# Kernel tuning notes

Hardware: AMD Instinct MI355X
Metric: run time of the kernel (lower is better)

The kernel has to match this reference:

```python
import jax, jax.numpy as jnp
import numpy as np

M, N, K = 35637, 15872, 20
FEAT = 128
EPS = 1e-5
W0 = 1.0  # Sine frequency


def setup_inputs() -> dict:
    key = jax.random.key(0)
    ks = jax.random.split(key, 8)
    x_feat = jax.random.normal(ks[0], (1, N, FEAT), dtype=jnp.float32)
    w_up_inputs = jax.random.uniform(ks[1], (1, 7, M, K), dtype=jnp.float32)
    idx = jax.random.randint(ks[2], (1, M, K), 0, N - 1)
    conv0_w = jax.random.normal(ks[3], (128, 7), dtype=jnp.float32) * (1.0 / np.sqrt(7))
    convs_w = jax.random.normal(ks[4], (7, 128, 128), dtype=jnp.float32) * (1.0 / np.sqrt(128))
    gammas = jnp.ones((8, 128), dtype=jnp.float32)
    betas = jnp.zeros((8, 128), dtype=jnp.float32)
    final_w = jax.random.normal(ks[5], (1, 128), dtype=jnp.float32) * (1.0 / np.sqrt(128))
    final_b = jnp.zeros((1,), dtype=jnp.float32)
    return {"x_feat": x_feat, "w_up_inputs": w_up_inputs, "idx": idx,
            "conv0_w": conv0_w, "convs_w": convs_w, "gammas": gammas,
            "betas": betas, "final_w": final_w, "final_b": final_b}


def _conv_bn_sine(h, W, g, b):
    # 1x1 conv == per-point matmul over channel dim; h: (B, M, K, Cin)
    h = jnp.einsum('bmkc,oc->bmko', h, W)
    # BatchNorm2d in training mode: batch stats over (B, M, K) per channel
    mu = jnp.mean(h, axis=(0, 1, 2))
    var = jnp.var(h, axis=(0, 1, 2))
    h = (h - mu) * jax.lax.rsqrt(var + EPS) * g + b
    return jnp.sin(W0 * h)


def reference(x_feat, w_up_inputs, idx, conv0_w, convs_w, gammas, betas, final_w, final_b):
    # w_up_inputs: (B, 7, M, K) -> channels-last (B, M, K, 7)
    h = jnp.transpose(w_up_inputs, (0, 2, 3, 1))
    h = _conv_bn_sine(h, conv0_w, gammas[0], betas[0])
    for i in range(7):
        h = _conv_bn_sine(h, convs_w[i], gammas[i + 1], betas[i + 1])
    # final 1x1 conv with bias -> logits (B, M, K, 1)
    logits = jnp.einsum('bmkc,oc->bmko', h, final_w) + final_b
    w = jax.nn.softmax(logits, axis=2)  # softmax over K neighbors
    # index_points: gather x_feat[b, idx[b, m, k], :] -> (B, M, K, FEAT)
    gathered = jax.vmap(lambda pts, ix: pts[ix])(x_feat, idx)
    feat_H = jnp.sum(w * gathered, axis=2)  # (B, M, FEAT)
    return feat_H
```

## Files before the change

kernel.cpp:

```cpp
#include <hip/hip_runtime.h>

#define PP 712740
#define MM 35637
#define KK 20
#define NF 15872
#define NTILES 44547
#define NSUPER 11137
#define ZROWS (NSUPER * 64)

typedef _Float16 h16;
typedef __attribute__((ext_vector_type(8))) _Float16 f16x8;
typedef __attribute__((ext_vector_type(4))) float f32x4;

__global__ __launch_bounds__(256) void k_zero(double* __restrict__ gs) {
  const int t = threadIdx.x;
#pragma unroll
  for (int i = 0; i < 8; ++i) gs[i * 256 + t] = 0.0;
}

__global__ __launch_bounds__(256) void k_stats0(
    const float* __restrict__ up,
    const float* __restrict__ w0,
    double* __restrict__ gs)
{
  __shared__ float w0s[128 * 7];
  __shared__ double red[4][256];
  const int t = threadIdx.x;
  for (int i = t; i < 128 * 7; i += 256) w0s[i] = (float)(h16)w0[i];
  __syncthreads();

  const int w = t >> 6;
  const int lane = t & 63;
  const int ln = lane & 15;
  const int q = lane >> 4;

  float sp[32], qp[32];
#pragma unroll
  for (int i = 0; i < 32; ++i) { sp[i] = 0.f; qp[i] = 0.f; }

  const int gw = blockIdx.x * 4 + w;
  for (int tile = gw; tile < NTILES; tile += gridDim.x * 4) {
    const int p = tile * 16 + ln;
    const bool act = p < PP;
    float u[7];
#pragma unroll
    for (int c7 = 0; c7 < 7; ++c7) u[c7] = act ? up[(size_t)c7 * PP + p] : 0.f;

#pragma unroll
    for (int ks = 0; ks < 4; ++ks)
#pragma unroll
      for (int j = 0; j < 8; ++j) {
        const int c = ks * 32 + q * 8 + j;
        float acc = 0.f;
#pragma unroll
        for (int c7 = 0; c7 < 7; ++c7) acc = fmaf(w0s[c * 7 + c7], u[c7], acc);
        const int si = ks * 8 + j;
        sp[si] += acc;
        qp[si] = fmaf(acc, acc, qp[si]);
      }
  }

#pragma unroll
  for (int i = 0; i < 32; ++i) {
#pragma unroll
    for (int d = 1; d < 16; d <<= 1) {
      sp[i] += __shfl_xor(sp[i], d, 64);
      qp[i] += __shfl_xor(qp[i], d, 64);
    }
  }
  if (ln == 0) {
#pragma unroll
    for (int ks = 0; ks < 4; ++ks)
#pragma unroll
      for (int j = 0; j < 8; ++j) {
        const int c = ks * 32 + q * 8 + j;
        red[w][c] = (double)sp[ks * 8 + j];
        red[w][128 + c] = (double)qp[ks * 8 + j];
      }
  }
  __syncthreads();
  double v = red[0][t] + red[1][t] + red[2][t] + red[3][t];
  atomicAdd(&gs[t], v);
}

__global__ __launch_bounds__(256, 3) void k_layer1(
    const float* __restrict__ up,
    const float* __restrict__ w0,
    h16* __restrict__ zout,
    const double* __restrict__ gsp,
    double* __restrict__ gso,
    const float* __restrict__ W,
    const float* __restrict__ gamma,
    const float* __restrict__ beta)
{
  __shared__ h16 actA[8192];
  __shared__ h16 actB[8192];
  __shared__ double red[256];

  const int t = threadIdx.x;
  const int w = t >> 6;
  const int lane = t & 63;
  const int ln = lane & 15;
  const int q = lane >> 4;
  const int G = (int)gridDim.x;

  float sc[8], sh[8];
  {
    const double n = (double)PP;
    const int cb = (t & 15) * 8;
#pragma unroll
    for (int j = 0; j < 8; ++j) {
      const int c = cb + j;
      const double mu = gsp[c] / n;
      const double var = gsp[128 + c] / n - mu * mu;
      const float rstd = (float)(1.0 / sqrt(var + 1e-5));
      sc[j] = rstd * gamma[c];
      sh[j] = beta[c] - (float)mu * sc[j];
    }
  }

  h16 w0h[7][8];
  {
    const int cb = (t & 15) * 8;
#pragma unroll
    for (int c7 = 0; c7 < 7; ++c7)
#pragma unroll
      for (int j = 0; j < 8; ++j)
        w0h[c7][j] = (h16)w0[(cb + j) * 7 + c7];
  }

  const int ob = w * 32;
  f16x8 wfr[2][4];
#pragma unroll
  for (int nt = 0; nt < 2; ++nt) {
    const int row_g = ob + (ln >> 2) * 8 + nt * 4 + (ln & 3);
    const float* wrow = W + (size_t)row_g * 128;
#pragma unroll
    for (int ks = 0; ks < 4; ++ks) {
      const float* src = wrow + ks * 32 + q * 8;
      const float4 aa = *(const float4*)src;
      const float4 bb = *(const float4*)(src + 4);
      f16x8 b;
      b[0] = (h16)aa.x; b[1] = (h16)aa.y; b[2] = (h16)aa.z; b[3] = (h16)aa.w;
      b[4] = (h16)bb.x; b[5] = (h16)bb.y; b[6] = (h16)bb.z; b[7] = (h16)bb.w;
      wfr[nt][ks] = b;
    }
  }

  float sp[8], qp[8];
#pragma unroll
  for (int i = 0; i < 8; ++i) { sp[i] = 0.f; qp[i] = 0.f; }

  const int wbase = (t >> 4) * 256 + (((t & 15) ^ ((t >> 4) & 7)) << 4);
  int raddr[4];
#pragma unroll
  for (int ks = 0; ks < 4; ++ks)
    raddr[ks] = ln * 256 + (((ks * 4 + q) ^ (ln & 7)) << 4);
  const int obase = ln * 256 + (((w * 4 + q) ^ (ln & 7)) << 4);
  const int rbase = (t >> 4) * 256 + (((t & 15) ^ ((t >> 4) & 7)) << 4);

  char* A = (char*)actA;
  char* B = (char*)actB;

  for (int stile = blockIdx.x; stile < NSUPER; stile += G) {
    float u[4][7];
#pragma unroll
    for (int s = 0; s < 4; ++s) {
      const int p = stile * 64 + (t >> 4) + 16 * s;
      const bool act = p < PP;
#pragma unroll
      for (int c7 = 0; c7 < 7; ++c7)
        u[s][c7] = act ? up[(size_t)c7 * PP + p] : 0.f;
    }

#pragma unroll
    for (int s = 0; s < 4; ++s) {
      f16x8 av;
#pragma unroll
      for (int j = 0; j < 8; ++j) {
        float acc = 0.f;
#pragma unroll
        for (int c7 = 0; c7 < 7; ++c7)
          acc = fmaf((float)w0h[c7][j], u[s][c7], acc);
        av[j] = (h16)__sinf(fmaf(acc, sc[j], sh[j]));
      }
      *(f16x8*)(A + (wbase + s * 4096)) = av;
    }

    asm volatile("s_waitcnt lgkmcnt(0)\n\ts_barrier" ::: "memory");

#pragma unroll
    for (int ot = 0; ot < 4; ++ot) {
      f16x8 afr[4];
#pragma unroll
      for (int ks = 0; ks < 4; ++ks)
        afr[ks] = *(const f16x8*)(A + (ot * 4096 + raddr[ks]));

      f32x4 acc0 = (f32x4){0.f, 0.f, 0.f, 0.f};
      f32x4 acc1 = (f32x4){0.f, 0.f, 0.f, 0.f};
#pragma unroll
      for (int ks = 0; ks < 4; ++ks) {
        acc0 = __builtin_amdgcn_mfma_f32_16x16x32_f16(wfr[0][ks], afr[ks], acc0, 0, 0, 0);
        acc1 = __builtin_amdgcn_mfma_f32_16x16x32_f16(wfr[1][ks], afr[ks], acc1, 0, 0, 0);
      }

      const int p = stile * 64 + ot * 16 + ln;
      if (p < PP) {
#pragma unroll
        for (int r = 0; r < 4; ++r) {
          sp[r]     += acc0[r];
          qp[r]      = fmaf(acc0[r], acc0[r], qp[r]);
          sp[4 + r] += acc1[r];
          qp[4 + r]  = fmaf(acc1[r], acc1[r], qp[4 + r]);
        }
      }
      f16x8 o;
      o[0] = (h16)acc0[0]; o[1] = (h16)acc0[1]; o[2] = (h16)acc0[2]; o[3] = (h16)acc0[3];
      o[4] = (h16)acc1[0]; o[5] = (h16)acc1[1]; o[6] = (h16)acc1[2]; o[7] = (h16)acc1[3];
      *(f16x8*)(B + (ot * 4096 + obase)) = o;
    }

    asm volatile("s_waitcnt lgkmcnt(0)\n\ts_barrier" ::: "memory");

    {
      const size_t zo = (size_t)stile * 8192;
#pragma unroll
      for (int pass = 0; pass < 4; ++pass) {
        const f16x8 v = *(const f16x8*)(B + (pass * 4096 + rbase));
        *(f16x8*)(zout + zo + (size_t)pass * 2048 + (size_t)t * 8) = v;
      }
    }
  }

#pragma unroll
  for (int i = 0; i < 8; ++i) {
#pragma unroll
    for (int d = 1; d < 16; d <<= 1) {
      sp[i] += __shfl_xor(sp[i], d, 64);
      qp[i] += __shfl_xor(qp[i], d, 64);
    }
  }
  if (ln == 0) {
#pragma unroll
    for (int r = 0; r < 4; ++r) {
      const int c = ob + q * 8 + r;
      red[c]           = (double)sp[r];
      red[c + 4]       = (double)sp[4 + r];
      red[128 + c]     = (double)qp[r];
      red[128 + c + 4] = (double)qp[4 + r];
    }
  }
  __syncthreads();
  atomicAdd(&gso[t], red[t]);
}

__global__ __launch_bounds__(256, 4) void k_layer(
    const h16* zin,
    h16* zout,
    const double* __restrict__ gsp,
    double* __restrict__ gso,
    const float* __restrict__ W,
    const float* __restrict__ gamma,
    const float* __restrict__ beta)
{
  __shared__ h16 actA[8192];
  __shared__ h16 actB[8192];
  __shared__ double red[256];

  const int t = threadIdx.x;
  const int w = t >> 6;
  const int lane = t & 63;
  const int ln = lane & 15;
  const int q = lane >> 4;
  const int G = (int)gridDim.x;

  float sc[8], sh[8];
  {
    const double n = (double)PP;
    const int cb = (t & 15) * 8;
#pragma unroll
    for (int j = 0; j < 8; ++j) {
      const int c = cb + j;
      const double mu = gsp[c] / n;
      const double var = gsp[128 + c] / n - mu * mu;
      const float rstd = (float)(1.0 / sqrt(var + 1e-5));
      sc[j] = rstd * gamma[c];
      sh[j] = beta[c] - (float)mu * sc[j];
    }
  }

  const int ob = w * 32;
  f16x8 wfr[2][4];
#pragma unroll
  for (int nt = 0; nt < 2; ++nt) {
    const int row_g = ob + (ln >> 2) * 8 + nt * 4 + (ln & 3);
    const float* wrow = W + (size_t)row_g * 128;
#pragma unroll
    for (int ks = 0; ks < 4; ++ks) {
      const float* src = wrow + ks * 32 + q * 8;
      const float4 aa = *(const float4*)src;
      const float4 bb = *(const float4*)(src + 4);
      f16x8 b;
      b[0] = (h16)aa.x; b[1] = (h16)aa.y; b[2] = (h16)aa.z; b[3] = (h16)aa.w;
      b[4] = (h16)bb.x; b[5] = (h16)bb.y; b[6] = (h16)bb.z; b[7] = (h16)bb.w;
      wfr[nt][ks] = b;
    }
  }

  float sp[8], qp[8];
#pragma unroll
  for (int i = 0; i < 8; ++i) { sp[i] = 0.f; qp[i] = 0.f; }

  const size_t roff = (size_t)(t >> 4) * 128 + (size_t)(t & 15) * 8;
  const int wbase = (t >> 4) * 256 + (((t & 15) ^ ((t >> 4) & 7)) << 4);
  int raddr[4];
#pragma unroll
  for (int ks = 0; ks < 4; ++ks)
    raddr[ks] = ln * 256 + (((ks * 4 + q) ^ (ln & 7)) << 4);
  const int obase = ln * 256 + (((w * 4 + q) ^ (ln & 7)) << 4);
  const int rbase = (t >> 4) * 256 + (((t & 15) ^ ((t >> 4) & 7)) << 4);

  int stile = blockIdx.x;
  f16x8 raw[4];
  {
    const h16* src = zin + (size_t)stile * 8192 + roff;
#pragma unroll
    for (int s = 0; s < 4; ++s) raw[s] = *(const f16x8*)(src + s * 2048);
  }

  char* A = (char*)actA;
  char* B = (char*)actB;

  for (; stile < NSUPER; stile += G) {
#pragma unroll
    for (int s = 0; s < 4; ++s) {
      f16x8 av;
#pragma unroll
      for (int j = 0; j < 8; ++j)
        av[j] = (h16)__sinf(fmaf((float)raw[s][j], sc[j], sh[j]));
      *(f16x8*)(A + (wbase + s * 4096)) = av;
    }

    {
      const int nxt = (stile + G < NSUPER) ? stile + G : NSUPER - 1;
      const h16* src = zin + (size_t)nxt * 8192 + roff;
#pragma unroll
      for (int s = 0; s < 4; ++s) raw[s] = *(const f16x8*)(src + s * 2048);
    }

    asm volatile("s_waitcnt lgkmcnt(0)\n\ts_barrier" ::: "memory");

#pragma unroll
    for (int ot = 0; ot < 4; ++ot) {
      f16x8 afr[4];
#pragma unroll
      for (int ks = 0; ks < 4; ++ks)
        afr[ks] = *(const f16x8*)(A + (ot * 4096 + raddr[ks]));

      f32x4 acc0 = (f32x4){0.f, 0.f, 0.f, 0.f};
      f32x4 acc1 = (f32x4){0.f, 0.f, 0.f, 0.f};
#pragma unroll
      for (int ks = 0; ks < 4; ++ks) {
        acc0 = __builtin_amdgcn_mfma_f32_16x16x32_f16(wfr[0][ks], afr[ks], acc0, 0, 0, 0);
        acc1 = __builtin_amdgcn_mfma_f32_16x16x32_f16(wfr[1][ks], afr[ks], acc1, 0, 0, 0);
      }

      const int p = stile * 64 + ot * 16 + ln;
      if (p < PP) {
#pragma unroll
        for (int r = 0; r < 4; ++r) {
          sp[r]     += acc0[r];
          qp[r]      = fmaf(acc0[r], acc0[r], qp[r]);
          sp[4 + r] += acc1[r];
          qp[4 + r]  = fmaf(acc1[r], acc1[r], qp[4 + r]);
        }
      }
      f16x8 o;
      o[0] = (h16)acc0[0]; o[1] = (h16)acc0[1]; o[2] = (h16)acc0[2]; o[3] = (h16)acc0[3];
      o[4] = (h16)acc1[0]; o[5] = (h16)acc1[1]; o[6] = (h16)acc1[2]; o[7] = (h16)acc1[3];
      *(f16x8*)(B + (ot * 4096 + obase)) = o;
    }

    asm volatile("s_waitcnt lgkmcnt(0)\n\ts_barrier" ::: "memory");

    {
      const size_t zo = (size_t)stile * 8192;
#pragma unroll
      for (int pass = 0; pass < 4; ++pass) {
        const f16x8 v = *(const f16x8*)(B + (pass * 4096 + rbase));
        *(f16x8*)(zout + zo + (size_t)pass * 2048 + (size_t)t * 8) = v;
      }
    }
  }

#pragma unroll
  for (int i = 0; i < 8; ++i) {
#pragma unroll
    for (int d = 1; d < 16; d <<= 1) {
      sp[i] += __shfl_xor(sp[i], d, 64);
      qp[i] += __shfl_xor(qp[i], d, 64);
    }
  }
  if (ln == 0) {
#pragma unroll
    for (int r = 0; r < 4; ++r) {
      const int c = ob + q * 8 + r;
      red[c]           = (double)sp[r];
      red[c + 4]       = (double)sp[4 + r];
      red[128 + c]     = (double)qp[r];
      red[128 + c + 4] = (double)qp[4 + r];
    }
  }
  __syncthreads();
  atomicAdd(&gso[t], red[t]);
}

__global__ __launch_bounds__(256) void k_outf(
    const h16* __restrict__ z,
    const double* __restrict__ gsp,
    const float* __restrict__ gamma,
    const float* __restrict__ beta,
    const float* __restrict__ fw,
    const float* __restrict__ fb,
    const int* __restrict__ idx,
    const float* __restrict__ xf,
    float* __restrict__ out)
{
  const int gw = (int)((blockIdx.x * 256 + threadIdx.x) >> 6);
  const int lane = (int)(threadIdx.x & 63);
  if (gw >= MM) return;
  const int m = gw;
  const int ln = lane & 15;
  const int q = lane >> 4;
  const int c0 = ln * 8;

  float scv[8], shv[8], fv[8];
#pragma unroll
  for (int j = 0; j < 8; ++j) {
    const int c = c0 + j;
    const double n = (double)PP;
    const double mu = gsp[c] / n;
    const double var = gsp[128 + c] / n - mu * mu;
    const float rstd = (float)(1.0 / sqrt(var + 1e-5));
    scv[j] = rstd * gamma[c];
    shv[j] = beta[c] - (float)mu * scv[j];
    fv[j] = fw[c];
  }
  const float fbv = fb[0];

  float lg[5];
#pragma unroll
  for (int g = 0; g < 5; ++g) {
    const h16* zp = z + (size_t)(m * KK + g * 4 + q) * 128 + c0;
    const f16x8 raw = *(const f16x8*)zp;
    float part = 0.f;
#pragma unroll
    for (int j = 0; j < 8; ++j)
      part = fmaf(fv[j], __sinf(fmaf((float)raw[j], scv[j], shv[j])), part);
    part += __shfl_xor(part, 1, 64);
    part += __shfl_xor(part, 2, 64);
    part += __shfl_xor(part, 4, 64);
    part += __shfl_xor(part, 8, 64);
    lg[g] = part + fbv;
  }

  float l1[5], l2[5], l3[5];
#pragma unroll
  for (int g = 0; g < 5; ++g) {
    l1[g] = __shfl_xor(lg[g], 16, 64);
    l2[g] = __shfl_xor(lg[g], 32, 64);
    l3[g] = __shfl_xor(l1[g], 32, 64);
  }

  float mx = lg[0];
#pragma unroll
  for (int g = 0; g < 5; ++g) {
    mx = fmaxf(mx, lg[g]); mx = fmaxf(mx, l1[g]);
    mx = fmaxf(mx, l2[g]); mx = fmaxf(mx, l3[g]);
  }
  float w0e[5], w1e[5], w2e[5], w3e[5];
  float ssum = 0.f;
#pragma unroll
  for (int g = 0; g < 5; ++g) {
    w0e[g] = __expf(lg[g] - mx); ssum += w0e[g];
    w1e[g] = __expf(l1[g] - mx); ssum += w1e[g];
    w2e[g] = __expf(l2[g] - mx); ssum += w2e[g];
    w3e[g] = __expf(l3[g] - mx); ssum += w3e[g];
  }
  const float inv = 1.f / ssum;

  float a0 = 0.f, a1 = 0.f;
#pragma unroll
  for (int g = 0; g < 5; ++g) {
#pragma unroll
    for (int e = 0; e < 4; ++e) {
      const int k = 4 * g + (q ^ e);
      const float we = (e == 0 ? w0e[g] : e == 1 ? w1e[g] : e == 2 ? w2e[g] : w3e[g]);
      const int r = idx[m * KK + k];
      const float wk = we * inv;
      a0 = fmaf(wk, xf[r * 128 + lane], a0);
      a1 = fmaf(wk, xf[r * 128 + 64 + lane], a1);
    }
  }
  out[m * 128 + lane] = a0;
  out[m * 128 + 64 + lane] = a1;
}

__global__ __launch_bounds__(256) void k_out(
    const float* __restrict__ logits,
    const int* __restrict__ idx,
    const float* __restrict__ xf,
    float* __restrict__ out)
{
  const int gw = (int)((blockIdx.x * 256 + threadIdx.x) >> 6);
  const int lane = threadIdx.x & 63;
  if (gw >= MM) return;
  const int m = gw;

  float l[KK];
#pragma unroll
  for (int k = 0; k < KK; ++k) l[k] = logits[m * KK + k];
  float mx = l[0];
#pragma unroll
  for (int k = 1; k < KK; ++k) mx = fmaxf(mx, l[k]);
  float ssum = 0.f;
#pragma unroll
  for (int k = 0; k < KK; ++k) { l[k] = __expf(l[k] - mx); ssum += l[k]; }
  const float inv = 1.f / ssum;

  float a0 = 0.f, a1 = 0.f;
#pragma unroll
  for (int k = 0; k < KK; ++k) {
    const int r = idx[m * KK + k];
    const float wk = l[k] * inv;
    a0 = fmaf(wk, xf[r * 128 + lane], a0);
    a1 = fmaf(wk, xf[r * 128 + 64 + lane], a1);
  }
  out[m * 128 + lane] = a0;
  out[m * 128 + 64 + lane] = a1;
}

__global__ __launch_bounds__(256) void k_chain(
    const float* __restrict__ up,
    const float* __restrict__ w0,
    const float* __restrict__ wc,
    const float* __restrict__ gam,
    const float* __restrict__ bet,
    const double* __restrict__ gs,
    double* __restrict__ gso,
    int jl, int mode,
    const float* __restrict__ fw,
    const float* __restrict__ fb,
    float* __restrict__ logits)
{
  __shared__ float sc_s[8][128], sh_s[8][128];
  __shared__ double bred[4][256];
  const int t = threadIdx.x;
  const int lane = t & 63;

  const int nbn = (mode == 0) ? jl : 8;
  for (int i = t; i < nbn * 128; i += 256) {
    const int L = i >> 7, c = i & 127;
    const double n = (double)PP;
    const double mu = gs[L * 256 + c] / n;
    const double var = gs[L * 256 + 128 + c] / n - mu * mu;
    const float rstd = (float)(1.0 / sqrt(var + 1e-5));
    const float sc = rstd * gam[L * 128 + c];
    sc_s[L][c] = sc;
    sh_s[L][c] = bet[L * 128 + c] - (float)mu * sc;
  }
  __syncthreads();

  double lS0 = 0, lS1 = 0, lQ0 = 0, lQ1 = 0;

  for (int p0 = blockIdx.x * 256; p0 < PP; p0 += gridDim.x * 256) {
    const int p = p0 + t;
    const bool act = p < PP;

    float a[128];
    {
      float u[7];
#pragma unroll
      for (int c = 0; c < 7; ++c) u[c] = act ? up[c * PP + p] : 0.f;
#pragma unroll 1
      for (int och = 0; och < 16; ++och) {
#pragma unroll
        for (int j = 0; j < 8; ++j) {
          float acc = 0.f;
#pragma unroll
          for (int c = 0; c < 7; ++c)
            acc = fmaf(w0[(och * 8 + j) * 7 + c], u[c], acc);
          a[och * 8 + j] = acc;
        }
      }
    }

#pragma unroll 1
    for (int L = 0; L < jl; ++L) {
#pragma unroll
      for (int c = 0; c < 128; ++c)
        a[c] = act ? __sinf(fmaf(a[c], sc_s[L][c], sh_s[L][c])) : 0.f;
      float b[128];
      const float* W = wc + (size_t)L * 128 * 128;
#pragma unroll 1
      for (int och = 0; och < 16; ++och) {
#pragma unroll
        for (int j = 0; j < 8; ++j) {
          float acc = 0.f;
#pragma unroll
          for (int c = 0; c < 128; ++c)
            acc = fmaf(W[(och * 8 + j) * 128 + c], a[c], acc);
          b[och * 8 + j] = acc;
        }
      }
#pragma unroll
      for (int c = 0; c < 128; ++c) a[c] = b[c];
    }

    if (mode == 0) {
#pragma unroll
      for (int o = 0; o < 128; ++o) {
        float s = a[o];
        float qv = a[o] * a[o];
#pragma unroll
        for (int d = 32; d > 0; d >>= 1) {
          s += __shfl_xor(s, d, 64);
          qv += __shfl_xor(qv, d, 64);
        }
        if ((o & 63) == lane) {
          if (o < 64) { lS0 += (double)s; lQ0 += (double)qv; }
          else        { lS1 += (double)s; lQ1 += (double)qv; }
        }
      }
    } else if (act) {
      float acc = fb[0];
#pragma unroll
      for (int c = 0; c < 128; ++c) {
        const float h = fmaf(a[c], sc_s[7][c], sh_s[7][c]);
        acc = fmaf(fw[c], __sinf(h), acc);
      }
      logits[p] = acc;
    }
  }

  if (mode == 0) {
    const int w = t >> 6;
    bred[w][lane]       = lS0;
    bred[w][64 + lane]  = lS1;
    bred[w][128 + lane] = lQ0;
    bred[w][192 + lane] = lQ1;
    __syncthreads();
    double v = bred[0][t] + bred[1][t] + bred[2][t] + bred[3][t];
    atomicAdd(&gso[t], v);
  }
}

extern "C" void kernel_launch(void* const* d_in, const int* in_sizes, int n_in,
                              void* d_out, int out_size, void* d_ws, size_t ws_size,
                              hipStream_t stream) {
  const float* xf  = (const float*)d_in[0];
  const float* up  = (const float*)d_in[1];
  const int*   idx = (const int*)d_in[2];
  const float* w0  = (const float*)d_in[3];
  const float* wc  = (const float*)d_in[4];
  const float* gam = (const float*)d_in[5];
  const float* bet = (const float*)d_in[6];
  const float* fw  = (const float*)d_in[7];
  const float* fb  = (const float*)d_in[8];
  float* out = (float*)d_out;

  char* ws = (char*)d_ws;
  const size_t zb     = (size_t)ZROWS * 128 * sizeof(h16);
  const size_t statsb = 8 * 256 * sizeof(double);
  const int NB = 1024;
  const int nbo = (MM + 3) / 4;

  if (ws_size >= zb + statsb) {
    h16* z = (h16*)ws;
    double* gs = (double*)(ws + zb);

    k_zero<<<1, 256, 0, stream>>>(gs);
    k_stats0<<<NB, 256, 0, stream>>>(up, w0, gs);
    k_layer1<<<NB, 256, 0, stream>>>(up, w0, z, gs, gs + 256,
                                     wc, gam, bet);
    for (int i = 2; i <= 7; ++i) {
      k_layer<<<NB, 256, 0, stream>>>(z, z,
                                      gs + (size_t)(i - 1) * 256,
                                      gs + (size_t)i * 256,
                                      wc + (size_t)(i - 1) * 128 * 128,
                                      gam + (size_t)(i - 1) * 128,
                                      bet + (size_t)(i - 1) * 128);
    }
    k_outf<<<nbo, 256, 0, stream>>>(z, gs + 7 * 256, gam + 7 * 128,
                                    bet + 7 * 128, fw, fb, idx, xf, out);
  } else {
    double* gs = (double*)ws;
    float* logits = (float*)(ws + statsb);

    k_zero<<<1, 256, 0, stream>>>(gs);
    for (int j = 0; j <= 7; ++j) {
      k_chain<<<NB, 256, 0, stream>>>(up, w0, wc, gam, bet, gs,
                                      gs + (size_t)j * 256, j, 0,
                                      fw, fb, logits);
    }
    k_chain<<<NB, 256, 0, stream>>>(up, w0, wc, gam, bet, gs,
                                    nullptr, 7, 1, fw, fb, logits);
    k_out<<<nbo, 256, 0, stream>>>(logits, idx, xf, out);
  }
}
```

Before: 708.6 us.

## Replace last layer write-back with stats-only pass plus recompute-to-logits pass

The final conv layer no longer writes its fp16 activations back to the workspace. One kernel computes the layer-7 matmul only to gather batch-norm statistics. A second kernel recomputes the same matmul, applies BN, sine and the final projection in registers, and writes only per-point logits. The existing k_out kernel then does the softmax and gather. This removes a full 712k×128 fp16 write and its later reread, at the cost of running the last matmul twice and launching one extra kernel.

```diff
diff --git a/kernel.cpp b/kernel.cpp
--- a/kernel.cpp
+++ b/kernel.cpp
@@ -415,95 +415,292 @@
   atomicAdd(&gso[t], red[t]);
 }
 
-__global__ __launch_bounds__(256) void k_outf(
-    const h16* __restrict__ z,
+__global__ __launch_bounds__(256, 4) void k_stats7(
+    const h16* __restrict__ zin,
     const double* __restrict__ gsp,
+    double* __restrict__ gso,
+    const float* __restrict__ W,
     const float* __restrict__ gamma,
-    const float* __restrict__ beta,
+    const float* __restrict__ beta)
+{
+  __shared__ h16 actA[8192];
+  __shared__ double red[256];
+
+  const int t = threadIdx.x;
+  const int w = t >> 6;
+  const int lane = t & 63;
+  const int ln = lane & 15;
+  const int q = lane >> 4;
+  const int G = (int)gridDim.x;
+
+  float sc[8], sh[8];
+  {
+    const double n = (double)PP;
+    const int cb = (t & 15) * 8;
+#pragma unroll
+    for (int j = 0; j < 8; ++j) {
+      const int c = cb + j;
+      const double mu = gsp[c] / n;
+      const double var = gsp[128 + c] / n - mu * mu;
+      const float rstd = (float)(1.0 / sqrt(var + 1e-5));
+      sc[j] = rstd * gamma[c];
+      sh[j] = beta[c] - (float)mu * sc[j];
+    }
+  }
+
+  const int ob = w * 32;
+  f16x8 wfr[2][4];
+#pragma unroll
+  for (int nt = 0; nt < 2; ++nt) {
+    const int row_g = ob + (ln >> 2) * 8 + nt * 4 + (ln & 3);
+    const float* wrow = W + (size_t)row_g * 128;
+#pragma unroll
+    for (int ks = 0; ks < 4; ++ks) {
+      const float* src = wrow + ks * 32 + q * 8;
+      const float4 aa = *(const float4*)src;
+      const float4 bb = *(const float4*)(src + 4);
+      f16x8 b;
+      b[0] = (h16)aa.x; b[1] = (h16)aa.y; b[2] = (h16)aa.z; b[3] = (h16)aa.w;
+      b[4] = (h16)bb.x; b[5] = (h16)bb.y; b[6] = (h16)bb.z; b[7] = (h16)bb.w;
+      wfr[nt][ks] = b;
+    }
+  }
+
+  float sp[8], qp[8];
+#pragma unroll
+  for (int i = 0; i < 8; ++i) { sp[i] = 0.f; qp[i] = 0.f; }
+
+  const size_t roff = (size_t)(t >> 4) * 128 + (size_t)(t & 15) * 8;
+  const int wbase = (t >> 4) * 256 + (((t & 15) ^ ((t >> 4) & 7)) << 4);
+  int raddr[4];
+#pragma unroll
+  for (int ks = 0; ks < 4; ++ks)
+    raddr[ks] = ln * 256 + (((ks * 4 + q) ^ (ln & 7)) << 4);
+
+  int stile = blockIdx.x;
+  f16x8 raw[4];
+  {
+    const h16* src = zin + (size_t)stile * 8192 + roff;
+#pragma unroll
+    for (int s = 0; s < 4; ++s) raw[s] = *(const f16x8*)(src + s * 2048);
+  }
+
+  char* A = (char*)actA;
+
+  for (; stile < NSUPER; stile += G) {
+#pragma unroll
+    for (int s = 0; s < 4; ++s) {
+      f16x8 av;
+#pragma unroll
+      for (int j = 0; j < 8; ++j)
+        av[j] = (h16)__sinf(fmaf((float)raw[s][j], sc[j], sh[j]));
+      *(f16x8*)(A + (wbase + s * 4096)) = av;
+    }
+
+    {
+      const int nxt = (stile + G < NSUPER) ? stile + G : NSUPER - 1;
+      const h16* src = zin + (size_t)nxt * 8192 + roff;
+#pragma unroll
+      for (int s = 0; s < 4; ++s) raw[s] = *(const f16x8*)(src + s * 2048);
+    }
+
+    asm volatile("s_waitcnt lgkmcnt(0)\n\ts_barrier" ::: "memory");
+
+#pragma unroll
+    for (int ot = 0; ot < 4; ++ot) {
+      f16x8 afr[4];
+#pragma unroll
+      for (int ks = 0; ks < 4; ++ks)
+        afr[ks] = *(const f16x8*)(A + (ot * 4096 + raddr[ks]));
+
+      f32x4 acc0 = (f32x4){0.f, 0.f, 0.f, 0.f};
+      f32x4 acc1 = (f32x4){0.f, 0.f, 0.f, 0.f};
+#pragma unroll
+      for (int ks = 0; ks < 4; ++ks) {
+        acc0 = __builtin_amdgcn_mfma_f32_16x16x32_f16(wfr[0][ks], afr[ks], acc0, 0, 0, 0);
+        acc1 = __builtin_amdgcn_mfma_f32_16x16x32_f16(wfr[1][ks], afr[ks], acc1, 0, 0, 0);
+      }
+
+      const int p = stile * 64 + ot * 16 + ln;
+      if (p < PP) {
+#pragma unroll
+        for (int r = 0; r < 4; ++r) {
+          sp[r]     += acc0[r];
+          qp[r]      = fmaf(acc0[r], acc0[r], qp[r]);
+          sp[4 + r] += acc1[r];
+          qp[4 + r]  = fmaf(acc1[r], acc1[r], qp[4 + r]);
+        }
+      }
+    }
+
+    asm volatile("s_waitcnt lgkmcnt(0)\n\ts_barrier" ::: "memory");
+  }
+
+#pragma unroll
+  for (int i = 0; i < 8; ++i) {
+#pragma unroll
+    for (int d = 1; d < 16; d <<= 1) {
+      sp[i] += __shfl_xor(sp[i], d, 64);
+      qp[i] += __shfl_xor(qp[i], d, 64);
+    }
+  }
+  if (ln == 0) {
+#pragma unroll
+    for (int r = 0; r < 4; ++r) {
+      const int c = ob + q * 8 + r;
+      red[c]           = (double)sp[r];
+      red[c + 4]       = (double)sp[4 + r];
+      red[128 + c]     = (double)qp[r];
+      red[128 + c + 4] = (double)qp[4 + r];
+    }
+  }
+  __syncthreads();
+  atomicAdd(&gso[t], red[t]);
+}
+
+__global__ __launch_bounds__(256, 3) void k_logits7(
+    const h16* __restrict__ zin,
+    const double* __restrict__ gspA,
+    const float* __restrict__ gamA,
+    const float* __restrict__ betA,
+    const float* __restrict__ W,
+    const double* __restrict__ gspO,
+    const float* __restrict__ gamO,
+    const float* __restrict__ betO,
     const float* __restrict__ fw,
     const float* __restrict__ fb,
-    const int* __restrict__ idx,
-    const float* __restrict__ xf,
-    float* __restrict__ out)
+    float* __restrict__ logits)
 {
-  const int gw = (int)((blockIdx.x * 256 + threadIdx.x) >> 6);
-  const int lane = (int)(threadIdx.x & 63);
-  if (gw >= MM) return;
-  const int m = gw;
+  __shared__ h16 actA[8192];
+  __shared__ float lf[4][64];
+
+  const int t = threadIdx.x;
+  const int w = t >> 6;
+  const int lane = t & 63;
   const int ln = lane & 15;
   const int q = lane >> 4;
-  const int c0 = ln * 8;
-
-  float scv[8], shv[8], fv[8];
-#pragma unroll
-  for (int j = 0; j < 8; ++j) {
-    const int c = c0 + j;
+  const int G = (int)gridDim.x;
+
+  float sc[8], sh[8];
+  {
     const double n = (double)PP;
-    const double mu = gsp[c] / n;
-    const double var = gsp[128 + c] / n - mu * mu;
-    const float rstd = (float)(1.0 / sqrt(var + 1e-5));
-    scv[j] = rstd * gamma[c];
-    shv[j] = beta[c] - (float)mu * scv[j];
-    fv[j] = fw[c];
+    const int cb = (t & 15) * 8;
+#pragma unroll
+    for (int j = 0; j < 8; ++j) {
+      const int c = cb + j;
+      const double mu = gspA[c] / n;
+      const double var = gspA[128 + c] / n - mu * mu;
+      const float rstd = (float)(1.0 / sqrt(var + 1e-5));
+      sc[j] = rstd * gamA[c];
+      sh[j] = betA[c] - (float)mu * sc[j];
+    }
+  }
+
+  const int ob = w * 32;
+  float scO[8], shO[8], fwO[8];
+  {
+    const double n = (double)PP;
+    const int cb = ob + q * 8;
+#pragma unroll
+    for (int j = 0; j < 8; ++j) {
+      const int c = cb + j;
+      const double mu = gspO[c] / n;
+      const double var = gspO[128 + c] / n - mu * mu;
+      const float rstd = (float)(1.0 / sqrt(var + 1e-5));
+      scO[j] = rstd * gamO[c];
+      shO[j] = betO[c] - (float)mu * scO[j];
+      fwO[j] = fw[c];
+    }
   }
   const float fbv = fb[0];
 
-  float lg[5];
-#pragma unroll
-  for (int g = 0; g < 5; ++g) {
-    const h16* zp = z + (size_t)(m * KK + g * 4 + q) * 128 + c0;
-    const f16x8 raw = *(const f16x8*)zp;
-    float part = 0.f;
-#pragma unroll
-    for (int j = 0; j < 8; ++j)
-      part = fmaf(fv[j], __sinf(fmaf((float)raw[j], scv[j], shv[j])), part);
-    part += __shfl_xor(part, 1, 64);
-    part += __shfl_xor(part, 2, 64);
-    part += __shfl_xor(part, 4, 64);
-    part += __shfl_xor(part, 8, 64);
-    lg[g] = part + fbv;
-  }
-
-  float l1[5], l2[5], l3[5];
-#pragma unroll
-  for (int g = 0; g < 5; ++g) {
-    l1[g] = __shfl_xor(lg[g], 16, 64);
-    l2[g] = __shfl_xor(lg[g], 32, 64);
-    l3[g] = __shfl_xor(l1[g], 32, 64);
-  }
-
-  float mx = lg[0];
-#pragma unroll
-  for (int g = 0; g < 5; ++g) {
-    mx = fmaxf(mx, lg[g]); mx = fmaxf(mx, l1[g]);
-    mx = fmaxf(mx, l2[g]); mx = fmaxf(mx, l3[g]);
-  }
-  float w0e[5], w1e[5], w2e[5], w3e[5];
-  float ssum = 0.f;
-#pragma unroll
-  for (int g = 0; g < 5; ++g) {
-    w0e[g] = __expf(lg[g] - mx); ssum += w0e[g];
-    w1e[g] = __expf(l1[g] - mx); ssum += w1e[g];
-    w2e[g] = __expf(l2[g] - mx); ssum += w2e[g];
-    w3e[g] = __expf(l3[g] - mx); ssum += w3e[g];
-  }
-  const float inv = 1.f / ssum;
-
-  float a0 = 0.f, a1 = 0.f;
-#pragma unroll
-  for (int g = 0; g < 5; ++g) {
-#pragma unroll
-    for (int e = 0; e < 4; ++e) {
-      const int k = 4 * g + (q ^ e);
-      const float we = (e == 0 ? w0e[g] : e == 1 ? w1e[g] : e == 2 ? w2e[g] : w3e[g]);
-      const int r = idx[m * KK + k];
-      const float wk = we * inv;
-      a0 = fmaf(wk, xf[r * 128 + lane], a0);
-      a1 = fmaf(wk, xf[r * 128 + 64 + lane], a1);
-    }
-  }
-  out[m * 128 + lane] = a0;
-  out[m * 128 + 64 + lane] = a1;
+  f16x8 wfr[2][4];
+#pragma unroll
+  for (int nt = 0; nt < 2; ++nt) {
+    const int row_g = ob + (ln >> 2) * 8 + nt * 4 + (ln & 3);
+    const float* wrow = W + (size_t)row_g * 128;
+#pragma unroll
+    for (int ks = 0; ks < 4; ++ks) {
+      const float* src = wrow + ks * 32 + q * 8;
+      const float4 aa = *(const float4*)src;
+      const float4 bb = *(const float4*)(src + 4);
+      f16x8 b;
+      b[0] = (h16)aa.x; b[1] = (h16)aa.y; b[2] = (h16)aa.z; b[3] = (h16)aa.w;
+      b[4] = (h16)bb.x; b[5] = (h16)bb.y; b[6] = (h16)bb.z; b[7] = (h16)bb.w;
+      wfr[nt][ks] = b;
+    }
+  }
+
+  const size_t roff = (size_t)(t >> 4) * 128 + (size_t)(t & 15) * 8;
+  const int wbase = (t >> 4) * 256 + (((t & 15) ^ ((t >> 4) & 7)) << 4);
+  int raddr[4];
+#pragma unroll
+  for (int ks = 0; ks < 4; ++ks)
+    raddr[ks] = ln * 256 + (((ks * 4 + q) ^ (ln & 7)) << 4);
+
+  int stile = blockIdx.x;
+  f16x8 raw[4];
+  {
+    const h16* src = zin + (size_t)stile * 8192 + roff;
+#pragma unroll
+    for (int s = 0; s < 4; ++s) raw[s] = *(const f16x8*)(src + s * 2048);
+  }
+
+  char* A = (char*)actA;
+
+  for (; stile < NSUPER; stile += G) {
+#pragma unroll
+    for (int s = 0; s < 4; ++s) {
+      f16x8 av;
+#pragma unroll
+      for (int j = 0; j < 8; ++j)
+        av[j] = (h16)__sinf(fmaf((float)raw[s][j], sc[j], sh[j]));
+      *(f16x8*)(A + (wbase + s * 4096)) = av;
+    }
+
+    {
+      const int nxt = (stile + G < NSUPER) ? stile + G : NSUPER - 1;
+      const h16* src = zin + (size_t)nxt * 8192 + roff;
+#pragma unroll
+      for (int s = 0; s < 4; ++s) raw[s] = *(const f16x8*)(src + s * 2048);
+    }
+
+    asm volatile("s_waitcnt lgkmcnt(0)\n\ts_barrier" ::: "memory");
+
+#pragma unroll
+    for (int ot = 0; ot < 4; ++ot) {
+      f16x8 afr[4];
+#pragma unroll
+      for (int ks = 0; ks < 4; ++ks)
+        afr[ks] = *(const f16x8*)(A + (ot * 4096 + raddr[ks]));
+
+      f32x4 acc0 = (f32x4){0.f, 0.f, 0.f, 0.f};
+      f32x4 acc1 = (f32x4){0.f, 0.f, 0.f, 0.f};
+#pragma unroll
+      for (int ks = 0; ks < 4; ++ks) {
+        acc0 = __builtin_amdgcn_mfma_f32_16x16x32_f16(wfr[0][ks], afr[ks], acc0, 0, 0, 0);
+        acc1 = __builtin_amdgcn_mfma_f32_16x16x32_f16(wfr[1][ks], afr[ks], acc1, 0, 0, 0);
+      }
+
+      float part = 0.f;
+#pragma unroll
+      for (int r = 0; r < 4; ++r) {
+        part = fmaf(fwO[r],     __sinf(fmaf(acc0[r], scO[r],     shO[r])),     part);
+        part = fmaf(fwO[4 + r], __sinf(fmaf(acc1[r], scO[4 + r], shO[4 + r])), part);
+      }
+      part += __shfl_xor(part, 16, 64);
+      part += __shfl_xor(part, 32, 64);
+      if (q == 0) lf[w][ot * 16 + ln] = part;
+    }
+
+    asm volatile("s_waitcnt lgkmcnt(0)\n\ts_barrier" ::: "memory");
+
+    if (t < 64) {
+      const int p = stile * 64 + t;
+      if (p < PP)
+        logits[p] = lf[0][t] + lf[1][t] + lf[2][t] + lf[3][t] + fbv;
+    }
+  }
 }
 
 __global__ __launch_bounds__(256) void k_out(
@@ -672,18 +869,20 @@
   char* ws = (char*)d_ws;
   const size_t zb     = (size_t)ZROWS * 128 * sizeof(h16);
   const size_t statsb = 8 * 256 * sizeof(double);
+  const size_t logb   = (size_t)PP * sizeof(float);
   const int NB = 1024;
   const int nbo = (MM + 3) / 4;
 
-  if (ws_size >= zb + statsb) {
+  if (ws_size >= zb + statsb + logb) {
     h16* z = (h16*)ws;
     double* gs = (double*)(ws + zb);
+    float* logits = (float*)(ws + zb + statsb);
 
     k_zero<<<1, 256, 0, stream>>>(gs);
     k_stats0<<<NB, 256, 0, stream>>>(up, w0, gs);
     k_layer1<<<NB, 256, 0, stream>>>(up, w0, z, gs, gs + 256,
                                      wc, gam, bet);
-    for (int i = 2; i <= 7; ++i) {
+    for (int i = 2; i <= 6; ++i) {
       k_layer<<<NB, 256, 0, stream>>>(z, z,
                                       gs + (size_t)(i - 1) * 256,
                                       gs + (size_t)i * 256,
@@ -691,8 +890,14 @@
                                       gam + (size_t)(i - 1) * 128,
                                       bet + (size_t)(i - 1) * 128);
     }
-    k_outf<<<nbo, 256, 0, stream>>>(z, gs + 7 * 256, gam + 7 * 128,
-                                    bet + 7 * 128, fw, fb, idx, xf, out);
+    k_stats7<<<NB, 256, 0, stream>>>(z, gs + 6 * 256, gs + 7 * 256,
+                                     wc + 6 * 128 * 128,
+                                     gam + 6 * 128, bet + 6 * 128);
+    k_logits7<<<NB, 256, 0, stream>>>(z, gs + 6 * 256, gam + 6 * 128,
+                                      bet + 6 * 128, wc + 6 * 128 * 128,
+                                      gs + 7 * 256, gam + 7 * 128,
+                                      bet + 7 * 128, fw, fb, logits);
+    k_out<<<nbo, 256, 0, stream>>>(logits, idx, xf, out);
   } else {
     double* gs = (double*)ws;
     float* logits = (float*)(ws + statsb);
```

After: 708.4 us. Within noise of the previous version (-0.0%).
